# Kernel tuning notes

Measured on AMD Instinct MI355X. Metric: run time of the kernel, lower is better.

The kernel has to match this reference:

```python
import jax, jax.numpy as jnp
import numpy as np

B, T, H, W = 2, 4, 32, 32
DINO_DIM, COG_DIM, NUM_HEADS = 768, 1920, 12
HEAD_DIM = DINO_DIM // NUM_HEADS


def _layernorm(x, g, b, eps=1e-5):
    mu = jnp.mean(x, axis=-1, keepdims=True)
    var = jnp.mean(jnp.square(x - mu), axis=-1, keepdims=True)
    return (x - mu) * jax.lax.rsqrt(var + eps) * g + b


def setup_inputs() -> dict:
    key = jax.random.key(0)
    ks = jax.random.split(key, 12)
    s_d = 1.0 / np.sqrt(DINO_DIM)
    s_c = 1.0 / np.sqrt(COG_DIM)
    return {
        "dino_query": jax.random.normal(ks[0], (B, DINO_DIM, H, W), jnp.float32),
        "cogvideo_keys": jax.random.normal(ks[1], (B, T, H, W, COG_DIM), jnp.float32),
        "temporal_weights": jax.random.uniform(ks[2], (T,), jnp.float32),
        "Wq": jax.random.normal(ks[3], (DINO_DIM, DINO_DIM), jnp.float32) * s_d,
        "bq": jnp.zeros((DINO_DIM,), jnp.float32),
        "Wk": jax.random.normal(ks[4], (COG_DIM, DINO_DIM), jnp.float32) * s_c,
        "bk": jnp.zeros((DINO_DIM,), jnp.float32),
        "Wv": jax.random.normal(ks[5], (COG_DIM, DINO_DIM), jnp.float32) * s_c,
        "bv": jnp.zeros((DINO_DIM,), jnp.float32),
        "Wo": jax.random.normal(ks[6], (DINO_DIM, DINO_DIM), jnp.float32) * s_d,
        "bo": jnp.zeros((DINO_DIM,), jnp.float32),
        "gq": jnp.ones((DINO_DIM,), jnp.float32),
        "Bq": jnp.zeros((DINO_DIM,), jnp.float32),
        "gkv": jnp.ones((COG_DIM,), jnp.float32),
        "Bkv": jnp.zeros((COG_DIM,), jnp.float32),
    }


def reference(dino_query, cogvideo_keys, temporal_weights,
              Wq, bq, Wk, bk, Wv, bv, Wo, bo, gq, Bq, gkv, Bkv):
    b, c, h, w = dino_query.shape
    t = cogvideo_keys.shape[1]
    hw, tkv = h * w, t * cogvideo_keys.shape[2] * cogvideo_keys.shape[3]

    # [B,C,H,W] -> [B,H,W,C]; project after LayerNorm
    xq = _layernorm(jnp.transpose(dino_query, (0, 2, 3, 1)), gq, Bq)
    xkv = _layernorm(cogvideo_keys, gkv, Bkv)
    q = xq @ Wq + bq                      # [B,H,W,C]
    k = xkv @ Wk + bk                     # [B,T,Hk,Wk,C]
    v = xkv @ Wv + bv

    q = q.reshape(b, hw, NUM_HEADS, HEAD_DIM).transpose(0, 2, 1, 3)    # [B,nh,HW,hd]
    k = k.reshape(b, tkv, NUM_HEADS, HEAD_DIM).transpose(0, 2, 1, 3)   # [B,nh,TKV,hd]
    v = v.reshape(b, tkv, NUM_HEADS, HEAD_DIM).transpose(0, 2, 1, 3)

    scores = jnp.einsum('bnqd,bnkd->bnqk', q, k) / np.sqrt(HEAD_DIM)   # [B,nh,HW,TKV]
    # per-key temporal weight: each of the T frames contributes HW keys
    w_key = jnp.repeat(temporal_weights, tkv // t)                     # [TKV]
    scores = scores * w_key[None, None, None, :]
    probs = jax.nn.softmax(scores, axis=-1)

    out = jnp.einsum('bnqk,bnkd->bnqd', probs, v)                      # [B,nh,HW,hd]
    out = out.transpose(0, 2, 1, 3).reshape(b, h, w, c)
    out = out @ Wo + bo
    return jnp.transpose(out, (0, 3, 1, 2))                            # [B,C,H,W]
```

## Files before the change

### kernel.cpp

```cpp
#include <hip/hip_runtime.h>
#include <hip/hip_bf16.h>
#include <math.h>

#define BB   2
#define HWl  1024
#define DINO 768
#define COG  1920
#define NHh  12
#define TKV  4096
#define MQ   (BB*HWl)
#define MKV  (BB*TKV)
#define NSPL 4
#define ROWS_PER_SPLIT (BB*NHh*HWl)

typedef __attribute__((ext_vector_type(8))) short bf16x8;
typedef __attribute__((ext_vector_type(4))) float f32x4;

__device__ __forceinline__ unsigned short f2bf_bits(float f) {
    __hip_bfloat16 h = __float2bfloat16(f);
    return *reinterpret_cast<unsigned short*>(&h);
}

__device__ __forceinline__ void glds16(const __hip_bfloat16* g, __hip_bfloat16* l) {
    __builtin_amdgcn_global_load_lds((const __attribute__((address_space(1))) void*)g,
                                     (__attribute__((address_space(3))) void*)l, 16, 0, 0);
}

__global__ void transpose_dino(const float* __restrict__ x, float* __restrict__ y) {
    int h0 = blockIdx.x * 64, c0 = blockIdx.y * 64, b = blockIdx.z;
    __shared__ float T[64][65];
    #pragma unroll
    for (int i = 0; i < 16; ++i) {
        int idx = threadIdx.x + i * 256;
        int c = idx >> 6, h = idx & 63;
        T[c][h] = x[((size_t)b * DINO + c0 + c) * HWl + h0 + h];
    }
    __syncthreads();
    #pragma unroll
    for (int i = 0; i < 16; ++i) {
        int idx = threadIdx.x + i * 256;
        int r = idx >> 6, c = idx & 63;
        y[((size_t)b * HWl + h0 + r) * DINO + c0 + c] = T[c][r];
    }
}

__global__ void ln_rows(const float* __restrict__ x, const float* __restrict__ g,
                        const float* __restrict__ be, __hip_bfloat16* __restrict__ y, int W) {
    int row = blockIdx.x, tid = threadIdx.x;
    int W4 = W >> 2;
    const float4* xr = (const float4*)(x + (size_t)row * W);
    const float4* g4 = (const float4*)g;
    const float4* b4 = (const float4*)be;
    int c0 = tid, c1 = tid + 256;
    bool p0 = c0 < W4, p1 = c1 < W4;
    float4 t0 = p0 ? xr[c0] : (float4){0.f,0.f,0.f,0.f};
    float4 t1 = p1 ? xr[c1] : (float4){0.f,0.f,0.f,0.f};
    float s  = t0.x + t0.y + t0.z + t0.w + t1.x + t1.y + t1.z + t1.w;
    float ss = t0.x*t0.x + t0.y*t0.y + t0.z*t0.z + t0.w*t0.w
             + t1.x*t1.x + t1.y*t1.y + t1.z*t1.z + t1.w*t1.w;
    __shared__ float rs_[256], rss_[256];
    rs_[tid] = s; rss_[tid] = ss;
    __syncthreads();
    for (int off = 128; off > 0; off >>= 1) {
        if (tid < off) { rs_[tid] += rs_[tid + off]; rss_[tid] += rss_[tid + off]; }
        __syncthreads();
    }
    __shared__ float smu, srstd;
    if (tid == 0) {
        float mu = rs_[0] / W;
        float var = rss_[0] / W - mu * mu;
        smu = mu; srstd = rsqrtf(var + 1e-5f);
    }
    __syncthreads();
    float mu = smu, rstd = srstd;
    ushort4* yr = (ushort4*)(y + (size_t)row * W);
    if (p0) {
        float4 gg = g4[c0], bb = b4[c0];
        ushort4 o;
        o.x = f2bf_bits((t0.x - mu) * rstd * gg.x + bb.x);
        o.y = f2bf_bits((t0.y - mu) * rstd * gg.y + bb.y);
        o.z = f2bf_bits((t0.z - mu) * rstd * gg.z + bb.z);
        o.w = f2bf_bits((t0.w - mu) * rstd * gg.w + bb.w);
        yr[c0] = o;
    }
    if (p1) {
        float4 gg = g4[c1], bb = b4[c1];
        ushort4 o;
        o.x = f2bf_bits((t1.x - mu) * rstd * gg.x + bb.x);
        o.y = f2bf_bits((t1.y - mu) * rstd * gg.y + bb.y);
        o.z = f2bf_bits((t1.z - mu) * rstd * gg.z + bb.z);
        o.w = f2bf_bits((t1.w - mu) * rstd * gg.w + bb.w);
        yr[c1] = o;
    }
}

__global__ void wt_trans(const float* __restrict__ Wq, const float* __restrict__ Wk,
                         const float* __restrict__ Wv, const float* __restrict__ Wo,
                         __hip_bfloat16* WqT, __hip_bfloat16* WkvT, __hip_bfloat16* WoT) {
    int mid = blockIdx.z;
    const float* src = (mid == 0) ? Wq : (mid == 1) ? Wk : (mid == 2) ? Wv : Wo;
    __hip_bfloat16* dst;
    int rowoff = 0;
    if (mid == 0) dst = WqT;
    else if (mid == 1) dst = WkvT;
    else if (mid == 2) { dst = WkvT; rowoff = 768; }
    else dst = WoT;
    int K = (mid == 1 || mid == 2) ? COG : DINO;
    int k0 = blockIdx.x * 32;
    if (k0 >= K) return;
    int n0 = blockIdx.y * 32;
    __shared__ float T[32][33];
    #pragma unroll
    for (int i = 0; i < 4; ++i) {
        int idx = threadIdx.x + i * 256;
        int r = idx >> 5, c = idx & 31;
        T[r][c] = src[(size_t)(k0 + r) * DINO + n0 + c];
    }
    __syncthreads();
    #pragma unroll
    for (int i = 0; i < 4; ++i) {
        int idx = threadIdx.x + i * 256;
        int r = idx >> 5, c = idx & 31;
        dst[(size_t)(rowoff + n0 + r) * K + k0 + c] = __float2bfloat16(T[c][r]);
    }
}

__global__ __launch_bounds__(256) void gemm_kv(const __hip_bfloat16* __restrict__ A,
                                               const __hip_bfloat16* __restrict__ Bt,
                                               const float* __restrict__ bk,
                                               const float* __restrict__ bv,
                                               __hip_bfloat16* __restrict__ kb,
                                               __hip_bfloat16* __restrict__ VT) {
    const int K = COG;
    __shared__ __hip_bfloat16 As[128 * 64];
    __shared__ __hip_bfloat16 Bs[128 * 64];
    int m0 = blockIdx.x * 128, n0 = blockIdx.y * 128;
    int tid = threadIdx.x, w = tid >> 6, lane = tid & 63;
    int l4 = lane & 15, lq = lane >> 4;
    int mq = (w & 1) * 64, nq = (w >> 1) * 64;
    f32x4 acc[4][4];
    #pragma unroll
    for (int i = 0; i < 4; ++i)
        #pragma unroll
        for (int j = 0; j < 4; ++j) acc[i][j] = (f32x4){0.f, 0.f, 0.f, 0.f};

    int rr = tid >> 3;
    int gc = (tid & 7) ^ (rr & 7);
    const __hip_bfloat16* ag = A  + (size_t)(m0 + rr) * K + gc * 8;
    const __hip_bfloat16* bg = Bt + (size_t)(n0 + rr) * K + gc * 8;
    __hip_bfloat16* asl = As + (w * 8) * 64;
    __hip_bfloat16* bsl = Bs + (w * 8) * 64;
    int sws = l4 & 7;

    for (int k0 = 0; k0 < K; k0 += 64) {
        __syncthreads();
        #pragma unroll
        for (int g = 0; g < 4; ++g) {
            glds16(ag + (size_t)(g * 32) * K + k0, asl + g * 32 * 64);
            glds16(bg + (size_t)(g * 32) * K + k0, bsl + g * 32 * 64);
        }
        __syncthreads();
        #pragma unroll
        for (int h = 0; h < 2; ++h) {
            bf16x8 a[4], b[4];
            #pragma unroll
            for (int i = 0; i < 4; ++i)
                a[i] = *(const bf16x8*)(As + (mq + 16 * i + l4) * 64 + (((h * 4 + lq) ^ sws) * 8));
            #pragma unroll
            for (int j = 0; j < 4; ++j)
                b[j] = *(const bf16x8*)(Bs + (nq + 16 * j + l4) * 64 + (((h * 4 + lq) ^ sws) * 8));
            #pragma unroll
            for (int i = 0; i < 4; ++i)
                #pragma unroll
                for (int j = 0; j < 4; ++j)
                    acc[i][j] = __builtin_amdgcn_mfma_f32_16x16x32_bf16(a[i], b[j], acc[i][j], 0, 0, 0);
        }
    }

    if (n0 < 768) {
        #pragma unroll
        for (int i = 0; i < 4; ++i)
            #pragma unroll
            for (int j = 0; j < 4; ++j)
                #pragma unroll
                for (int r = 0; r < 4; ++r) {
                    int m = m0 + mq + 16 * i + lq * 4 + r;
                    int n = n0 + nq + 16 * j + l4;
                    kb[(size_t)m * DINO + n] = __float2bfloat16(acc[i][j][r] + bk[n]);
                }
    } else {
        #pragma unroll
        for (int i = 0; i < 4; ++i)
            #pragma unroll
            for (int j = 0; j < 4; ++j)
                #pragma unroll
                for (int r = 0; r < 4; ++r) {
                    int m = m0 + mq + 16 * i + lq * 4 + r;
                    int n = n0 + nq + 16 * j + l4 - 768;
                    VT[((size_t)((m >> 12) * 768 + n)) * TKV + (m & 4095)] =
                        __float2bfloat16(acc[i][j][r] + bv[n]);
                }
    }
}

template<bool ONCHW>
__global__ __launch_bounds__(256) void gemm_qo(const __hip_bfloat16* __restrict__ A,
                                               const __hip_bfloat16* __restrict__ Bt,
                                               const float* __restrict__ bias,
                                               void* __restrict__ outp) {
    const int K = DINO;
    __shared__ __hip_bfloat16 As[64 * 64];
    __shared__ __hip_bfloat16 Bs[128 * 64];
    int m0 = blockIdx.x * 64, n0 = blockIdx.y * 128;
    int tid = threadIdx.x, w = tid >> 6, lane = tid & 63;
    int l4 = lane & 15, lq = lane >> 4;
    int mq = (w & 1) * 32, nq = (w >> 1) * 64;
    f32x4 acc[2][4];
    #pragma unroll
    for (int i = 0; i < 2; ++i)
        #pragma unroll
        for (int j = 0; j < 4; ++j) acc[i][j] = (f32x4){0.f, 0.f, 0.f, 0.f};

    int rr = tid >> 3;
    int gc = (tid & 7) ^ (rr & 7);
    const __hip_bfloat16* ag = A  + (size_t)(m0 + rr) * K + gc * 8;
    const __hip_bfloat16* bg = Bt + (size_t)(n0 + rr) * K + gc * 8;
    __hip_bfloat16* asl = As + (w * 8) * 64;
    __hip_bfloat16* bsl = Bs + (w * 8) * 64;
    int sws = l4 & 7;

    for (int k0 = 0; k0 < K; k0 += 64) {
        __syncthreads();
        #pragma unroll
        for (int g = 0; g < 2; ++g)
            glds16(ag + (size_t)(g * 32) * K + k0, asl + g * 32 * 64);
        #pragma unroll
        for (int g = 0; g < 4; ++g)
            glds16(bg + (size_t)(g * 32) * K + k0, bsl + g * 32 * 64);
        __syncthreads();
        #pragma unroll
        for (int h = 0; h < 2; ++h) {
            bf16x8 a[2], b[4];
            #pragma unroll
            for (int i = 0; i < 2; ++i)
                a[i] = *(const bf16x8*)(As + (mq + 16 * i + l4) * 64 + (((h * 4 + lq) ^ sws) * 8));
            #pragma unroll
            for (int j = 0; j < 4; ++j)
                b[j] = *(const bf16x8*)(Bs + (nq + 16 * j + l4) * 64 + (((h * 4 + lq) ^ sws) * 8));
            #pragma unroll
            for (int i = 0; i < 2; ++i)
                #pragma unroll
                for (int j = 0; j < 4; ++j)
                    acc[i][j] = ONCHW
                      ? __builtin_amdgcn_mfma_f32_16x16x32_bf16(b[j], a[i], acc[i][j], 0, 0, 0)
                      : __builtin_amdgcn_mfma_f32_16x16x32_bf16(a[i], b[j], acc[i][j], 0, 0, 0);
        }
    }

    if (!ONCHW) {
        __hip_bfloat16* out = (__hip_bfloat16*)outp;
        #pragma unroll
        for (int i = 0; i < 2; ++i)
            #pragma unroll
            for (int j = 0; j < 4; ++j)
                #pragma unroll
                for (int r = 0; r < 4; ++r) {
                    int m = m0 + mq + 16 * i + lq * 4 + r;
                    int n = n0 + nq + 16 * j + l4;
                    out[(size_t)m * DINO + n] = __float2bfloat16(acc[i][j][r] + bias[n]);
                }
    } else {
        float* out = (float*)outp;
        #pragma unroll
        for (int i = 0; i < 2; ++i)
            #pragma unroll
            for (int j = 0; j < 4; ++j)
                #pragma unroll
                for (int r = 0; r < 4; ++r) {
                    int n = n0 + nq + 16 * j + lq * 4 + r;
                    int m = m0 + mq + 16 * i + l4;
                    int b = m >> 10, hw = m & 1023;
                    out[((size_t)b * DINO + n) * HWl + hw] = acc[i][j][r] + bias[n];
                }
    }
}

__global__ __launch_bounds__(256) void attn2(const __hip_bfloat16* __restrict__ qb,
                                             const __hip_bfloat16* __restrict__ kb,
                                             const __hip_bfloat16* __restrict__ VT,
                                             const float* __restrict__ tw,
                                             float* __restrict__ Opart,
                                             float* __restrict__ lpart) {
    int bid = blockIdx.x;
    int g = bid % 96, qc = bid / 96;
    int s = g & 3, bh = g >> 2;
    int head = bh % NHh, b = bh / NHh;
    int tid = threadIdx.x, w = tid >> 6, lane = tid & 63;
    int l4 = lane & 15, lq = lane >> 4;

    __shared__ __hip_bfloat16 Ks[64 * 64];
    __shared__ __hip_bfloat16 Vs[64 * 64];
    __shared__ __hip_bfloat16 Ps[4 * 16 * 64];

    const __hip_bfloat16* qrow = qb + (size_t)(b * HWl + qc * 64 + w * 16 + l4) * DINO + head * 64;
    bf16x8 q0 = *(const bf16x8*)(qrow + lq * 8);
    bf16x8 q1 = *(const bf16x8*)(qrow + 32 + lq * 8);

    float wscale = tw[s] * 0.125f;
    float l_i = 0.f;
    f32x4 o[4];
    #pragma unroll
    for (int j = 0; j < 4; ++j) o[j] = (f32x4){0.f, 0.f, 0.f, 0.f};

    int rowA = w * 16 + (lane >> 3);
    int cg = (lane & 7) ^ ((lane >> 3) & 7);
    const __hip_bfloat16* kg0 = kb + (size_t)(b * TKV + s * 1024 + rowA) * DINO + head * 64 + cg * 8;
    const __hip_bfloat16* kg1 = kg0 + (size_t)8 * DINO;
    const __hip_bfloat16* vg0 = VT + (size_t)(b * 768 + head * 64 + rowA) * TKV + s * 1024 + cg * 8;
    const __hip_bfloat16* vg1 = vg0 + (size_t)8 * TKV;
    __hip_bfloat16* kl0 = Ks + (w * 2 + 0) * 512;
    __hip_bfloat16* kl1 = Ks + (w * 2 + 1) * 512;
    __hip_bfloat16* vl0 = Vs + (w * 2 + 0) * 512;
    __hip_bfloat16* vl1 = Vs + (w * 2 + 1) * 512;

    int sw0 = (lq ^ (l4 & 7)) * 8;
    int sw1 = ((4 + lq) ^ (l4 & 7)) * 8;

    for (int kt = 0; kt < 16; ++kt) {
        __syncthreads();
        glds16(kg0 + (size_t)kt * 64 * DINO, kl0);
        glds16(kg1 + (size_t)kt * 64 * DINO, kl1);
        glds16(vg0 + kt * 64, vl0);
        glds16(vg1 + kt * 64, vl1);
        __syncthreads();

        f32x4 st[4];
        #pragma unroll
        for (int j = 0; j < 4; ++j) {
            const __hip_bfloat16* kr = Ks + (16 * j + l4) * 64;
            bf16x8 kf0 = *(const bf16x8*)(kr + sw0);
            bf16x8 kf1 = *(const bf16x8*)(kr + sw1);
            f32x4 a = (f32x4){0.f, 0.f, 0.f, 0.f};
            a = __builtin_amdgcn_mfma_f32_16x16x32_bf16(kf0, q0, a, 0, 0, 0);
            a = __builtin_amdgcn_mfma_f32_16x16x32_bf16(kf1, q1, a, 0, 0, 0);
            st[j] = a;
        }

        float lsum = 0.f;
        #pragma unroll
        for (int j = 0; j < 4; ++j)
            #pragma unroll
            for (int r = 0; r < 4; ++r) {
                float e = __expf(st[j][r] * wscale);
                st[j][r] = e; lsum += e;
            }
        lsum += __shfl_xor(lsum, 16);
        lsum += __shfl_xor(lsum, 32);
        l_i += lsum;

        #pragma unroll
        for (int j = 0; j < 4; ++j) {
            ushort4 pk;
            pk.x = f2bf_bits(st[j][0]); pk.y = f2bf_bits(st[j][1]);
            pk.z = f2bf_bits(st[j][2]); pk.w = f2bf_bits(st[j][3]);
            int off = w * 1024 + l4 * 64 + (((2 * j + (lq >> 1)) ^ (l4 & 7)) << 3) + (lq & 1) * 4;
            *(ushort4*)&Ps[off] = pk;
        }
        bf16x8 pa0 = *(const bf16x8*)(Ps + w * 1024 + l4 * 64 + sw0);
        bf16x8 pa1 = *(const bf16x8*)(Ps + w * 1024 + l4 * 64 + sw1);

        #pragma unroll
        for (int j = 0; j < 4; ++j) {
            const __hip_bfloat16* vr = Vs + (16 * j + l4) * 64;
            bf16x8 vf0 = *(const bf16x8*)(vr + sw0);
            bf16x8 vf1 = *(const bf16x8*)(vr + sw1);
            o[j] = __builtin_amdgcn_mfma_f32_16x16x32_bf16(pa0, vf0, o[j], 0, 0, 0);
            o[j] = __builtin_amdgcn_mfma_f32_16x16x32_bf16(pa1, vf1, o[j], 0, 0, 0);
        }
    }

    size_t rowbase = (size_t)s * ROWS_PER_SPLIT + (size_t)(b * NHh + head) * HWl + qc * 64 + w * 16;
    #pragma unroll
    for (int j = 0; j < 4; ++j)
        #pragma unroll
        for (int r = 0; r < 4; ++r)
            Opart[(rowbase + lq * 4 + r) * 64 + j * 16 + l4] = o[j][r];
    if (lq == 0) lpart[rowbase + l4] = l_i;
}

__global__ void combine(const float* __restrict__ Opart, const float* __restrict__ lpart,
                        __hip_bfloat16* __restrict__ attn) {
    int p = blockIdx.x * 4 + (threadIdx.x >> 6);
    int d = threadIdx.x & 63;
    float L = 0.f, O = 0.f;
    #pragma unroll
    for (int s = 0; s < NSPL; ++s) {
        L += lpart[(size_t)s * ROWS_PER_SPLIT + p];
        O += Opart[((size_t)s * ROWS_PER_SPLIT + p) * 64 + d];
    }
    float res = O / L;
    int q = p & 1023;
    int bh = p >> 10;
    int head = bh % NHh, b = bh / NHh;
    attn[((size_t)(b * HWl + q)) * DINO + head * 64 + d] = __float2bfloat16(res);
}

extern "C" void kernel_launch(void* const* d_in, const int* in_sizes, int n_in,
                              void* d_out, int out_size, void* d_ws, size_t ws_size,
                              hipStream_t stream) {
    (void)in_sizes; (void)n_in; (void)out_size; (void)ws_size;
    const float* dino = (const float*)d_in[0];
    const float* cog  = (const float*)d_in[1];
    const float* tw   = (const float*)d_in[2];
    const float* Wq   = (const float*)d_in[3];
    const float* bq   = (const float*)d_in[4];
    const float* Wk   = (const float*)d_in[5];
    const float* bk   = (const float*)d_in[6];
    const float* Wv   = (const float*)d_in[7];
    const float* bv   = (const float*)d_in[8];
    const float* Wo   = (const float*)d_in[9];
    const float* bo   = (const float*)d_in[10];
    const float* gq   = (const float*)d_in[11];
    const float* Bq   = (const float*)d_in[12];
    const float* gkv  = (const float*)d_in[13];
    const float* Bkv  = (const float*)d_in[14];

    char* p = (char*)d_ws;
    float* xqT = (float*)p;                    p += (size_t)MQ * DINO * 4;
    __hip_bfloat16* xq = (__hip_bfloat16*)p;   p += (size_t)MQ * DINO * 2;
    char* alias = p;                           p += (size_t)MKV * COG * 2;
    __hip_bfloat16* xkv = (__hip_bfloat16*)alias;
    __hip_bfloat16* WqT  = (__hip_bfloat16*)p; p += (size_t)DINO * DINO * 2;
    __hip_bfloat16* WkvT = (__hip_bfloat16*)p; p += (size_t)1536 * COG * 2;
    __hip_bfloat16* WoT  = (__hip_bfloat16*)p; p += (size_t)DINO * DINO * 2;
    __hip_bfloat16* qb   = (__hip_bfloat16*)p; p += (size_t)MQ  * DINO * 2;
    __hip_bfloat16* kb   = (__hip_bfloat16*)p; p += (size_t)MKV * DINO * 2;
    __hip_bfloat16* VT   = (__hip_bfloat16*)p; p += (size_t)MKV * DINO * 2;
    __hip_bfloat16* attnb = (__hip_bfloat16*)p; p += (size_t)MQ * DINO * 2;
    float* Opart = (float*)alias;
    float* lpart = (float*)(alias + (size_t)NSPL * ROWS_PER_SPLIT * 64 * 4);

    transpose_dino<<<dim3(16, 12, 2), 256, 0, stream>>>(dino, xqT);
    ln_rows<<<MQ,  256, 0, stream>>>(xqT, gq, Bq, xq, DINO);
    ln_rows<<<MKV, 256, 0, stream>>>(cog, gkv, Bkv, xkv, COG);
    wt_trans<<<dim3(60, 24, 4), 256, 0, stream>>>(Wq, Wk, Wv, Wo, WqT, WkvT, WoT);

    gemm_qo<false><<<dim3(32, 6), 256, 0, stream>>>(xq, WqT, bq, qb);
    gemm_kv<<<dim3(64, 12), 256, 0, stream>>>(xkv, WkvT, bk, bv, kb, VT);

    attn2<<<BB * NHh * 16 * NSPL, 256, 0, stream>>>(qb, kb, VT, tw, Opart, lpart);
    combine<<<ROWS_PER_SPLIT / 4, 256, 0, stream>>>(Opart, lpart, attnb);

    gemm_qo<true><<<dim3(32, 6), 256, 0, stream>>>(attnb, WoT, bo, d_out);
}
```

Before: 293.1 us.

## Double query rows per attention wave and use warp-per-row LayerNorm

The attention kernel now has each wave handle 32 query rows instead of 16, reusing every K/V fragment loaded from shared memory for two MFMA chains. That halves the grid and the K/V global-to-LDS traffic per query, at the cost of more registers and a larger P buffer. Softmax exponentials switch to exp2f with the log2e factor folded into the scale. LayerNorm becomes one wavefront per row with shuffle reductions instead of a block-wide shared-memory tree with many barriers.

```diff
diff --git a/kernel.cpp b/kernel.cpp
--- a/kernel.cpp
+++ b/kernel.cpp
@@ -44,53 +44,46 @@
     }
 }
 
-__global__ void ln_rows(const float* __restrict__ x, const float* __restrict__ g,
-                        const float* __restrict__ be, __hip_bfloat16* __restrict__ y, int W) {
-    int row = blockIdx.x, tid = threadIdx.x;
-    int W4 = W >> 2;
+template<int W, int NC>
+__global__ void ln_rows_w(const float* __restrict__ x, const float* __restrict__ g,
+                          const float* __restrict__ be, __hip_bfloat16* __restrict__ y) {
+    const int W4 = W >> 2;
+    int row = blockIdx.x * 4 + (threadIdx.x >> 6);
+    int lane = threadIdx.x & 63;
     const float4* xr = (const float4*)(x + (size_t)row * W);
     const float4* g4 = (const float4*)g;
     const float4* b4 = (const float4*)be;
-    int c0 = tid, c1 = tid + 256;
-    bool p0 = c0 < W4, p1 = c1 < W4;
-    float4 t0 = p0 ? xr[c0] : (float4){0.f,0.f,0.f,0.f};
-    float4 t1 = p1 ? xr[c1] : (float4){0.f,0.f,0.f,0.f};
-    float s  = t0.x + t0.y + t0.z + t0.w + t1.x + t1.y + t1.z + t1.w;
-    float ss = t0.x*t0.x + t0.y*t0.y + t0.z*t0.z + t0.w*t0.w
-             + t1.x*t1.x + t1.y*t1.y + t1.z*t1.z + t1.w*t1.w;
-    __shared__ float rs_[256], rss_[256];
-    rs_[tid] = s; rss_[tid] = ss;
-    __syncthreads();
-    for (int off = 128; off > 0; off >>= 1) {
-        if (tid < off) { rs_[tid] += rs_[tid + off]; rss_[tid] += rss_[tid + off]; }
-        __syncthreads();
-    }
-    __shared__ float smu, srstd;
-    if (tid == 0) {
-        float mu = rs_[0] / W;
-        float var = rss_[0] / W - mu * mu;
-        smu = mu; srstd = rsqrtf(var + 1e-5f);
-    }
-    __syncthreads();
-    float mu = smu, rstd = srstd;
+    float4 v[NC];
+    float s = 0.f, ss = 0.f;
+    #pragma unroll
+    for (int i = 0; i < NC; ++i) {
+        int c = lane + i * 64;
+        float4 t = (c < W4) ? xr[c] : (float4){0.f, 0.f, 0.f, 0.f};
+        v[i] = t;
+        s  += t.x + t.y + t.z + t.w;
+        ss += t.x * t.x + t.y * t.y + t.z * t.z + t.w * t.w;
+    }
+    #pragma unroll
+    for (int off = 1; off < 64; off <<= 1) {
+        s  += __shfl_xor(s, off);
+        ss += __shfl_xor(ss, off);
+    }
+    float mu = s / W;
+    float rstd = rsqrtf(ss / W - mu * mu + 1e-5f);
     ushort4* yr = (ushort4*)(y + (size_t)row * W);
-    if (p0) {
-        float4 gg = g4[c0], bb = b4[c0];
-        ushort4 o;
-        o.x = f2bf_bits((t0.x - mu) * rstd * gg.x + bb.x);
-        o.y = f2bf_bits((t0.y - mu) * rstd * gg.y + bb.y);
-        o.z = f2bf_bits((t0.z - mu) * rstd * gg.z + bb.z);
-        o.w = f2bf_bits((t0.w - mu) * rstd * gg.w + bb.w);
-        yr[c0] = o;
-    }
-    if (p1) {
-        float4 gg = g4[c1], bb = b4[c1];
-        ushort4 o;
-        o.x = f2bf_bits((t1.x - mu) * rstd * gg.x + bb.x);
-        o.y = f2bf_bits((t1.y - mu) * rstd * gg.y + bb.y);
-        o.z = f2bf_bits((t1.z - mu) * rstd * gg.z + bb.z);
-        o.w = f2bf_bits((t1.w - mu) * rstd * gg.w + bb.w);
-        yr[c1] = o;
+    #pragma unroll
+    for (int i = 0; i < NC; ++i) {
+        int c = lane + i * 64;
+        if (c < W4) {
+            float4 t = v[i];
+            float4 gg = g4[c], bb = b4[c];
+            ushort4 o;
+            o.x = f2bf_bits((t.x - mu) * rstd * gg.x + bb.x);
+            o.y = f2bf_bits((t.y - mu) * rstd * gg.y + bb.y);
+            o.z = f2bf_bits((t.z - mu) * rstd * gg.z + bb.z);
+            o.w = f2bf_bits((t.w - mu) * rstd * gg.w + bb.w);
+            yr[c] = o;
+        }
     }
 }
 
@@ -285,7 +278,7 @@
     }
 }
 
-__global__ __launch_bounds__(256) void attn2(const __hip_bfloat16* __restrict__ qb,
+__global__ __launch_bounds__(256) void attn3(const __hip_bfloat16* __restrict__ qb,
                                              const __hip_bfloat16* __restrict__ kb,
                                              const __hip_bfloat16* __restrict__ VT,
                                              const float* __restrict__ tw,
@@ -300,17 +293,20 @@
 
     __shared__ __hip_bfloat16 Ks[64 * 64];
     __shared__ __hip_bfloat16 Vs[64 * 64];
-    __shared__ __hip_bfloat16 Ps[4 * 16 * 64];
-
-    const __hip_bfloat16* qrow = qb + (size_t)(b * HWl + qc * 64 + w * 16 + l4) * DINO + head * 64;
-    bf16x8 q0 = *(const bf16x8*)(qrow + lq * 8);
-    bf16x8 q1 = *(const bf16x8*)(qrow + 32 + lq * 8);
-
-    float wscale = tw[s] * 0.125f;
-    float l_i = 0.f;
-    f32x4 o[4];
-    #pragma unroll
-    for (int j = 0; j < 4; ++j) o[j] = (f32x4){0.f, 0.f, 0.f, 0.f};
+    __shared__ __hip_bfloat16 Ps[4 * 32 * 64];
+
+    const __hip_bfloat16* qbase = qb + (size_t)(b * HWl + qc * 128 + w * 32 + l4) * DINO + head * 64;
+    bf16x8 qA0 = *(const bf16x8*)(qbase + lq * 8);
+    bf16x8 qA1 = *(const bf16x8*)(qbase + 32 + lq * 8);
+    const __hip_bfloat16* qbase2 = qbase + (size_t)16 * DINO;
+    bf16x8 qB0 = *(const bf16x8*)(qbase2 + lq * 8);
+    bf16x8 qB1 = *(const bf16x8*)(qbase2 + 32 + lq * 8);
+
+    float c = tw[s] * 0.125f * 1.44269504f;
+    float l_iA = 0.f, l_iB = 0.f;
+    f32x4 oA[4], oB[4];
+    #pragma unroll
+    for (int j = 0; j < 4; ++j) { oA[j] = (f32x4){0.f,0.f,0.f,0.f}; oB[j] = (f32x4){0.f,0.f,0.f,0.f}; }
 
     int rowA = w * 16 + (lane >> 3);
     int cg = (lane & 7) ^ ((lane >> 3) & 7);
@@ -325,6 +321,8 @@
 
     int sw0 = (lq ^ (l4 & 7)) * 8;
     int sw1 = ((4 + lq) ^ (l4 & 7)) * 8;
+    __hip_bfloat16* PsA = Ps + w * 2048 + l4 * 64;
+    __hip_bfloat16* PsB = Ps + w * 2048 + (16 + l4) * 64;
 
     for (int kt = 0; kt < 16; ++kt) {
         __syncthreads();
@@ -334,58 +332,76 @@
         glds16(vg1 + kt * 64, vl1);
         __syncthreads();
 
-        f32x4 st[4];
+        f32x4 stA[4], stB[4];
         #pragma unroll
         for (int j = 0; j < 4; ++j) {
             const __hip_bfloat16* kr = Ks + (16 * j + l4) * 64;
             bf16x8 kf0 = *(const bf16x8*)(kr + sw0);
             bf16x8 kf1 = *(const bf16x8*)(kr + sw1);
-            f32x4 a = (f32x4){0.f, 0.f, 0.f, 0.f};
-            a = __builtin_amdgcn_mfma_f32_16x16x32_bf16(kf0, q0, a, 0, 0, 0);
-            a = __builtin_amdgcn_mfma_f32_16x16x32_bf16(kf1, q1, a, 0, 0, 0);
-            st[j] = a;
-        }
-
-        float lsum = 0.f;
+            f32x4 a = (f32x4){0.f,0.f,0.f,0.f};
+            a = __builtin_amdgcn_mfma_f32_16x16x32_bf16(kf0, qA0, a, 0, 0, 0);
+            a = __builtin_amdgcn_mfma_f32_16x16x32_bf16(kf1, qA1, a, 0, 0, 0);
+            stA[j] = a;
+            f32x4 bb = (f32x4){0.f,0.f,0.f,0.f};
+            bb = __builtin_amdgcn_mfma_f32_16x16x32_bf16(kf0, qB0, bb, 0, 0, 0);
+            bb = __builtin_amdgcn_mfma_f32_16x16x32_bf16(kf1, qB1, bb, 0, 0, 0);
+            stB[j] = bb;
+        }
+
+        float lsA = 0.f, lsB = 0.f;
         #pragma unroll
         for (int j = 0; j < 4; ++j)
             #pragma unroll
             for (int r = 0; r < 4; ++r) {
-                float e = __expf(st[j][r] * wscale);
-                st[j][r] = e; lsum += e;
+                float eA = exp2f(stA[j][r] * c);
+                float eB = exp2f(stB[j][r] * c);
+                stA[j][r] = eA; lsA += eA;
+                stB[j][r] = eB; lsB += eB;
             }
-        lsum += __shfl_xor(lsum, 16);
-        lsum += __shfl_xor(lsum, 32);
-        l_i += lsum;
+        lsA += __shfl_xor(lsA, 16); lsA += __shfl_xor(lsA, 32);
+        lsB += __shfl_xor(lsB, 16); lsB += __shfl_xor(lsB, 32);
+        l_iA += lsA; l_iB += lsB;
 
         #pragma unroll
         for (int j = 0; j < 4; ++j) {
-            ushort4 pk;
-            pk.x = f2bf_bits(st[j][0]); pk.y = f2bf_bits(st[j][1]);
-            pk.z = f2bf_bits(st[j][2]); pk.w = f2bf_bits(st[j][3]);
-            int off = w * 1024 + l4 * 64 + (((2 * j + (lq >> 1)) ^ (l4 & 7)) << 3) + (lq & 1) * 4;
-            *(ushort4*)&Ps[off] = pk;
-        }
-        bf16x8 pa0 = *(const bf16x8*)(Ps + w * 1024 + l4 * 64 + sw0);
-        bf16x8 pa1 = *(const bf16x8*)(Ps + w * 1024 + l4 * 64 + sw1);
+            int off = (((2 * j + (lq >> 1)) ^ (l4 & 7)) << 3) + (lq & 1) * 4;
+            ushort4 pA, pB;
+            pA.x = f2bf_bits(stA[j][0]); pA.y = f2bf_bits(stA[j][1]);
+            pA.z = f2bf_bits(stA[j][2]); pA.w = f2bf_bits(stA[j][3]);
+            pB.x = f2bf_bits(stB[j][0]); pB.y = f2bf_bits(stB[j][1]);
+            pB.z = f2bf_bits(stB[j][2]); pB.w = f2bf_bits(stB[j][3]);
+            *(ushort4*)&PsA[off] = pA;
+            *(ushort4*)&PsB[off] = pB;
+        }
+        bf16x8 paA0 = *(const bf16x8*)(PsA + sw0);
+        bf16x8 paA1 = *(const bf16x8*)(PsA + sw1);
+        bf16x8 paB0 = *(const bf16x8*)(PsB + sw0);
+        bf16x8 paB1 = *(const bf16x8*)(PsB + sw1);
 
         #pragma unroll
         for (int j = 0; j < 4; ++j) {
             const __hip_bfloat16* vr = Vs + (16 * j + l4) * 64;
             bf16x8 vf0 = *(const bf16x8*)(vr + sw0);
             bf16x8 vf1 = *(const bf16x8*)(vr + sw1);
-            o[j] = __builtin_amdgcn_mfma_f32_16x16x32_bf16(pa0, vf0, o[j], 0, 0, 0);
-            o[j] = __builtin_amdgcn_mfma_f32_16x16x32_bf16(pa1, vf1, o[j], 0, 0, 0);
-        }
-    }
-
-    size_t rowbase = (size_t)s * ROWS_PER_SPLIT + (size_t)(b * NHh + head) * HWl + qc * 64 + w * 16;
+            oA[j] = __builtin_amdgcn_mfma_f32_16x16x32_bf16(paA0, vf0, oA[j], 0, 0, 0);
+            oA[j] = __builtin_amdgcn_mfma_f32_16x16x32_bf16(paA1, vf1, oA[j], 0, 0, 0);
+            oB[j] = __builtin_amdgcn_mfma_f32_16x16x32_bf16(paB0, vf0, oB[j], 0, 0, 0);
+            oB[j] = __builtin_amdgcn_mfma_f32_16x16x32_bf16(paB1, vf1, oB[j], 0, 0, 0);
+        }
+    }
+
+    size_t rb = (size_t)s * ROWS_PER_SPLIT + (size_t)(b * NHh + head) * HWl + qc * 128 + w * 32;
     #pragma unroll
     for (int j = 0; j < 4; ++j)
         #pragma unroll
-        for (int r = 0; r < 4; ++r)
-            Opart[(rowbase + lq * 4 + r) * 64 + j * 16 + l4] = o[j][r];
-    if (lq == 0) lpart[rowbase + l4] = l_i;
+        for (int r = 0; r < 4; ++r) {
+            Opart[(rb + lq * 4 + r) * 64 + j * 16 + l4]      = oA[j][r];
+            Opart[(rb + 16 + lq * 4 + r) * 64 + j * 16 + l4] = oB[j][r];
+        }
+    if (lq == 0) {
+        lpart[rb + l4]      = l_iA;
+        lpart[rb + 16 + l4] = l_iB;
+    }
 }
 
 __global__ void combine(const float* __restrict__ Opart, const float* __restrict__ lpart,
@@ -441,14 +457,14 @@
     float* lpart = (float*)(alias + (size_t)NSPL * ROWS_PER_SPLIT * 64 * 4);
 
     transpose_dino<<<dim3(16, 12, 2), 256, 0, stream>>>(dino, xqT);
-    ln_rows<<<MQ,  256, 0, stream>>>(xqT, gq, Bq, xq, DINO);
-    ln_rows<<<MKV, 256, 0, stream>>>(cog, gkv, Bkv, xkv, COG);
+    ln_rows_w<DINO, 3><<<MQ / 4,  256, 0, stream>>>(xqT, gq, Bq, xq);
+    ln_rows_w<COG,  8><<<MKV / 4, 256, 0, stream>>>(cog, gkv, Bkv, xkv);
     wt_trans<<<dim3(60, 24, 4), 256, 0, stream>>>(Wq, Wk, Wv, Wo, WqT, WkvT, WoT);
 
     gemm_qo<false><<<dim3(32, 6), 256, 0, stream>>>(xq, WqT, bq, qb);
     gemm_kv<<<dim3(64, 12), 256, 0, stream>>>(xkv, WkvT, bk, bv, kb, VT);
 
-    attn2<<<BB * NHh * 16 * NSPL, 256, 0, stream>>>(qb, kb, VT, tw, Opart, lpart);
+    attn3<<<BB * NHh * 8 * NSPL, 256, 0, stream>>>(qb, kb, VT, tw, Opart, lpart);
     combine<<<ROWS_PER_SPLIT / 4, 256, 0, stream>>>(Opart, lpart, attnb);
 
     gemm_qo<true><<<dim3(32, 6), 256, 0, stream>>>(attnb, WoT, bo, d_out);
```

Result: no change. 295.7 us (+0.9%).
